# Kernel optimization log

Measured on AMD Instinct MI355X. Metric: run time of the kernel, lower is better.

Reference implementation:

```python
import jax, jax.numpy as jnp
import numpy as np

B, N, C, H = 8, 2048, 512, 8
D = C // H                      # head dim = 64
Q_LENGTHS = [1024 + 128 * i for i in range(B)]  # ragged: 1024..1920, sum below
TQ = sum(Q_LENGTHS)             # 11776 total queries


def setup_inputs() -> dict:
    key = jax.random.key(0)
    ks = jax.random.split(key, 5)
    w = 0.02  # init scale for weights
    return {
        "x": jax.random.normal(ks[0], (B, N, C), jnp.float32),
        "q": jax.random.normal(ks[1], (TQ, C), jnp.float32),
        "Wq": jax.random.normal(ks[2], (C, C), jnp.float32) * w,
        "Wkv": jax.random.normal(ks[3], (2 * C, C), jnp.float32) * w,
        "Wproj": jax.random.normal(ks[4], (C, C), jnp.float32) * w,
        "bproj": jnp.zeros((C,), jnp.float32),
        "q_lengths": jnp.array(Q_LENGTHS, jnp.int32),
        "max_q_len": max(Q_LENGTHS),
    }


def reference(x, q, Wq, Wkv, Wproj, bproj, q_lengths, max_q_len):
    # Eval path of Attention.forward: batched_sparse_attention(q, k, v, q_lengths, scale)
    # == varlen cross-attention: queries of batch b attend over all N kv tokens of batch b.
    Tq = q.shape[0]
    scale = D ** -0.5

    qh = (q @ Wq.T).reshape(Tq, H, D)                 # [Tq, H, D]
    kv = (x @ Wkv.T).reshape(B, N, 2, H, D)
    k = kv[:, :, 0]                                   # [B, N, H, D]
    v = kv[:, :, 1]                                   # [B, N, H, D]

    # ragged -> padded per-batch layout
    csum = jnp.cumsum(q_lengths)                      # [B]
    offs = jnp.concatenate([jnp.zeros((1,), csum.dtype), csum])
    tok = jnp.arange(Tq)
    q_batch = (tok[:, None] >= csum[None, :]).sum(-1)  # [Tq] batch id per query
    q_pos = tok - offs[q_batch]                        # [Tq] position within batch

    qpad = jnp.zeros((B, max_q_len, H, D), qh.dtype).at[q_batch, q_pos].set(qh)

    scores = jnp.einsum('blhd,bnhd->bhln', qpad, k) * scale  # [B, H, L, N]
    attn = jax.nn.softmax(scores, axis=-1)                   # all N keys valid
    out = jnp.einsum('bhln,bnhd->blhd', attn, v)             # [B, L, H, D]

    out = out[q_batch, q_pos].reshape(Tq, C)           # gather ragged rows back
    return out @ Wproj.T + bproj
```

## Files before the change

kernel.cpp:

```cpp
#include <hip/hip_runtime.h>
#include <hip/hip_bf16.h>
#include <math.h>

constexpr int Cc = 512;
constexpr int Hh = 8;
constexpr int Dd = 64;
constexpr int Nn = 2048;
constexpr int Bb = 8;
constexpr int GK = 512;

typedef __attribute__((ext_vector_type(8))) short short8;
typedef __attribute__((ext_vector_type(4))) float f32x4;
typedef __attribute__((ext_vector_type(4))) unsigned int u32x4;
typedef __attribute__((ext_vector_type(2))) unsigned int u32x2;

#define C2SCALE 0.1803368801f

static __device__ __forceinline__ ushort f2bf(float v) {
  __hip_bfloat16 h = __float2bfloat16(v);
  return *reinterpret_cast<ushort*>(&h);
}
static __device__ __forceinline__ float bf2f(ushort u) {
  __hip_bfloat16 h = *reinterpret_cast<__hip_bfloat16*>(&u);
  return __bfloat162float(h);
}
static __device__ __forceinline__ unsigned int pk2(float f0, float f1) {
  return (unsigned int)f2bf(f0) | ((unsigned int)f2bf(f1) << 16);
}

template <int MODE, int TERMS, bool AF32, bool BF32>
__global__ __launch_bounds__(256) void mfma_nt2_kernel(
    const void* __restrict__ A0p, const void* __restrict__ A1p,
    const void* __restrict__ B0p, const void* __restrict__ B1p,
    const float* __restrict__ bias, float* __restrict__ Cf,
    ushort* __restrict__ Chi, int Nc)
{
  __shared__ ushort lAh[128 * 32];
  __shared__ ushort lBh[128 * 32];
  __shared__ ushort lAl[TERMS == 3 ? 128 * 32 : 1];
  __shared__ ushort lBl[TERMS == 3 ? 128 * 32 : 1];

  const int tid = threadIdx.x;
  const int w = tid >> 6, lane = tid & 63;
  const int c = lane & 15, g = lane >> 4;
  const int wr = (w >> 1) * 64, wc = (w & 1) * 64;
  const int m0 = blockIdx.y * 128, n0 = blockIdx.x * 128;
  const int sr = tid >> 2;
  const int sk = (tid & 3) * 8;

  short8 rAh[2], rAl[2], rBh[2], rBl[2];

  auto ldf32 = [&](const float* F, size_t idx, short8& h, short8& l) {
    const float4 f0 = *(const float4*)(F + idx);
    const float4 f1 = *(const float4*)(F + idx + 4);
    const float vv[8] = {f0.x, f0.y, f0.z, f0.w, f1.x, f1.y, f1.z, f1.w};
#pragma unroll
    for (int j = 0; j < 8; ++j) {
      const ushort hb = f2bf(vv[j]);
      ((ushort*)&h)[j] = hb;
      if (TERMS == 3) ((ushort*)&l)[j] = f2bf(vv[j] - bf2f(hb));
    }
  };

  auto loadA = [&](int k0) {
#pragma unroll
    for (int hf = 0; hf < 2; ++hf) {
      const size_t idx = (size_t)(m0 + sr + hf * 64) * GK + k0 + sk;
      if (AF32) {
        ldf32((const float*)A0p, idx, rAh[hf], rAl[hf]);
      } else {
        rAh[hf] = *(const short8*)((const ushort*)A0p + idx);
        if (TERMS == 3) rAl[hf] = *(const short8*)((const ushort*)A1p + idx);
      }
    }
  };
  auto loadB = [&](int k0) {
#pragma unroll
    for (int hf = 0; hf < 2; ++hf) {
      const size_t idx = (size_t)(n0 + sr + hf * 64) * GK + k0 + sk;
      if (BF32) {
        ldf32((const float*)B0p, idx, rBh[hf], rBl[hf]);
      } else {
        rBh[hf] = *(const short8*)((const ushort*)B0p + idx);
        if (TERMS == 3) rBl[hf] = *(const short8*)((const ushort*)B1p + idx);
      }
    }
  };

  f32x4 acc[4][4] = {};
  loadA(0);
  loadB(0);

  for (int k0 = 0; k0 < GK; k0 += 32) {
    __syncthreads();
    *(short8*)&lAh[sr * 32 + sk]        = rAh[0];
    *(short8*)&lAh[(sr + 64) * 32 + sk] = rAh[1];
    *(short8*)&lBh[sr * 32 + sk]        = rBh[0];
    *(short8*)&lBh[(sr + 64) * 32 + sk] = rBh[1];
    if (TERMS == 3) {
      *(short8*)&lAl[sr * 32 + sk]        = rAl[0];
      *(short8*)&lAl[(sr + 64) * 32 + sk] = rAl[1];
      *(short8*)&lBl[sr * 32 + sk]        = rBl[0];
      *(short8*)&lBl[(sr + 64) * 32 + sk] = rBl[1];
    }
    __syncthreads();
    if (k0 + 32 < GK) { loadA(k0 + 32); loadB(k0 + 32); }

    short8 ah[4], al[4], bh[4], bl[4];
#pragma unroll
    for (int i = 0; i < 4; ++i) {
      const int ar = (wr + i * 16 + c) * 32 + g * 8;
      const int br = (wc + i * 16 + c) * 32 + g * 8;
      ah[i] = *(const short8*)&lAh[ar];
      bh[i] = *(const short8*)&lBh[br];
      if (TERMS == 3) {
        al[i] = *(const short8*)&lAl[ar];
        bl[i] = *(const short8*)&lBl[br];
      }
    }
#pragma unroll
    for (int mi = 0; mi < 4; ++mi)
#pragma unroll
      for (int nj = 0; nj < 4; ++nj) {
        if (TERMS == 3) {
          acc[mi][nj] = __builtin_amdgcn_mfma_f32_16x16x32_bf16(ah[mi], bl[nj], acc[mi][nj], 0,0,0);
          acc[mi][nj] = __builtin_amdgcn_mfma_f32_16x16x32_bf16(al[mi], bh[nj], acc[mi][nj], 0,0,0);
        }
        acc[mi][nj] = __builtin_amdgcn_mfma_f32_16x16x32_bf16(ah[mi], bh[nj], acc[mi][nj], 0,0,0);
      }
  }

#pragma unroll
  for (int mi = 0; mi < 4; ++mi) {
#pragma unroll
    for (int r = 0; r < 4; ++r) {
      const size_t rb = (size_t)(m0 + wr + mi * 16 + g * 4 + r) * Nc;
#pragma unroll
      for (int nj = 0; nj < 4; ++nj) {
        const int col = n0 + wc + nj * 16 + c;
        const float v = acc[mi][nj][r];
        if (MODE == 0) {
          Cf[rb + col] = v + bias[col];
        } else if (MODE == 1) {
          Chi[rb + col] = f2bf(v);
        } else {
          Chi[rb + col] = f2bf(v * C2SCALE);
        }
      }
    }
  }
}

__global__ __launch_bounds__(256, 2) void mfma_kv_fused_kernel(
    const float* __restrict__ x, const float* __restrict__ Wkv,
    ushort* __restrict__ kbf, ushort* __restrict__ vtb, int BN)
{
  __shared__ ushort smem[128 * 136];
  ushort* lA   = smem;
  ushort* lBk  = smem + 128 * 32;
  ushort* lBv  = smem + 2 * 128 * 32;
  ushort* tbuf = smem;

  const int tid = threadIdx.x;
  const int w = tid >> 6, lane = tid & 63;
  const int c = lane & 15, g = lane >> 4;
  const int wr = (w >> 1) * 64, wc = (w & 1) * 64;
  const int n0 = blockIdx.x * 128, m0 = blockIdx.y * 128;
  const int sr = tid >> 2, sk = (tid & 3) * 8;

  auto cvt8 = [&](const float* F, size_t idx) -> short8 {
    const float4 f0 = *(const float4*)(F + idx);
    const float4 f1 = *(const float4*)(F + idx + 4);
    const float vv[8] = {f0.x, f0.y, f0.z, f0.w, f1.x, f1.y, f1.z, f1.w};
    short8 h;
#pragma unroll
    for (int j = 0; j < 8; ++j) ((ushort*)&h)[j] = f2bf(vv[j]);
    return h;
  };

  short8 rA[2], rBk[2], rBv[2];
  auto loadAll = [&](int k0) {
#pragma unroll
    for (int hf = 0; hf < 2; ++hf) {
      rA[hf]  = cvt8(x,   (size_t)(m0 + sr + hf * 64) * GK + k0 + sk);
      rBk[hf] = cvt8(Wkv, (size_t)(n0 + sr + hf * 64) * GK + k0 + sk);
      rBv[hf] = cvt8(Wkv, (size_t)(512 + n0 + sr + hf * 64) * GK + k0 + sk);
    }
  };

  f32x4 ak[4][4] = {};
  f32x4 av[4][4] = {};
  loadAll(0);

  for (int k0 = 0; k0 < GK; k0 += 32) {
    __syncthreads();
    *(short8*)&lA[sr * 32 + sk]         = rA[0];
    *(short8*)&lA[(sr + 64) * 32 + sk]  = rA[1];
    *(short8*)&lBk[sr * 32 + sk]        = rBk[0];
    *(short8*)&lBk[(sr + 64) * 32 + sk] = rBk[1];
    *(short8*)&lBv[sr * 32 + sk]        = rBv[0];
    *(short8*)&lBv[(sr + 64) * 32 + sk] = rBv[1];
    __syncthreads();
    if (k0 + 32 < GK) loadAll(k0 + 32);

    short8 a[4], bk[4], bv[4];
#pragma unroll
    for (int i = 0; i < 4; ++i) {
      const int ar = (wr + i * 16 + c) * 32 + g * 8;
      const int br = (wc + i * 16 + c) * 32 + g * 8;
      a[i]  = *(const short8*)&lA[ar];
      bk[i] = *(const short8*)&lBk[br];
      bv[i] = *(const short8*)&lBv[br];
    }
#pragma unroll
    for (int mi = 0; mi < 4; ++mi)
#pragma unroll
      for (int nj = 0; nj < 4; ++nj) {
        ak[mi][nj] = __builtin_amdgcn_mfma_f32_16x16x32_bf16(a[mi], bk[nj], ak[mi][nj], 0,0,0);
        av[mi][nj] = __builtin_amdgcn_mfma_f32_16x16x32_bf16(a[mi], bv[nj], av[mi][nj], 0,0,0);
      }
  }

#pragma unroll
  for (int mi = 0; mi < 4; ++mi)
#pragma unroll
    for (int r = 0; r < 4; ++r) {
      const size_t rb = (size_t)(m0 + wr + mi * 16 + g * 4 + r) * Cc;
#pragma unroll
      for (int nj = 0; nj < 4; ++nj)
        kbf[rb + n0 + wc + nj * 16 + c] = f2bf(ak[mi][nj][r]);
    }

  __syncthreads();
#pragma unroll
  for (int mi = 0; mi < 4; ++mi)
#pragma unroll
    for (int r = 0; r < 4; ++r) {
      const int tl = wr + mi * 16 + g * 4 + r;
#pragma unroll
      for (int nj = 0; nj < 4; ++nj) {
        const int dl = wc + nj * 16 + c;
        tbuf[dl * 136 + tl] = f2bf(av[mi][nj][r]);
      }
    }
  __syncthreads();
#pragma unroll
  for (int it = 0; it < 8; ++it) {
    const int idx = tid + it * 256;
    const int row = idx >> 4;
    const int c8 = (idx & 15) * 8;
    *(short8*)&vtb[(size_t)(n0 + row) * BN + m0 + c8] =
        *(const short8*)&tbuf[row * 136 + c8];
  }
}

__global__ __launch_bounds__(256, 4) void attn_mfma12_kernel(
    const ushort* __restrict__ qhi,
    const ushort* __restrict__ kbf,
    const ushort* __restrict__ vtb,
    ushort* __restrict__ ohi,
    ushort* __restrict__ olo)
{
  constexpr int QOFF[8] = {0, 1024, 2176, 3456, 4864, 6400, 8064, 9856};

  const int lin = blockIdx.x;
  const int b  = lin & 7;
  const int h  = (lin >> 3) & 7;
  const int qt = lin >> 6;

  const int Lb  = 1024 + 128 * b;
  const int off = QOFF[b];
  if (qt * 128 >= Lb) return;

  constexpr int KP = 72;
  constexpr int VP = 136;
  constexpr int NC = Nn / 128;
  __shared__ ushort Ks[128 * KP];
  __shared__ ushort Vs[64 * VP];

  const int tid = threadIdx.x;
  const int lane = tid & 63;
  const int w = tid >> 6;
  const int c = lane & 15;
  const int g = (lane >> 4) & 3;

  short8 qf[2][2];
  int qrow[2];
#pragma unroll
  for (int t = 0; t < 2; ++t) {
    qrow[t] = off + qt * 128 + w * 32 + t * 16 + c;
    const size_t base = (size_t)qrow[t] * Cc + h * Dd + g * 8;
    qf[t][0] = *(const short8*)(qhi + base);
    qf[t][1] = *(const short8*)(qhi + base + 32);
  }

  float l_part[2] = {0.f, 0.f};
  f32x4 accO4[2][4] = {};

  const size_t kbase = (size_t)b * Nn * Cc + h * Dd;
  const size_t vbase = (size_t)h * Dd * (Bb * Nn) + (size_t)b * Nn;

  for (int ch = 0; ch < NC; ++ch) {
    __syncthreads();
#pragma unroll
    for (int it = 0; it < 4; ++it) {
      const int i = tid + it * 256;
      const int row = i >> 3, c8 = (i & 7) * 8;
      *(short8*)&Ks[row * KP + c8] =
          *(const short8*)&kbf[kbase + (size_t)(ch * 128 + row) * Cc + c8];
    }
#pragma unroll
    for (int it = 0; it < 4; ++it) {
      const int i = tid + it * 256;
      const int row = i >> 4, c8 = (i & 15) * 8;
      const int kb1 = (c8 & ~31) | (((c8 >> 3) & 3) << 2);
      const size_t gb = vbase + (size_t)row * (Bb * Nn) + ch * 128;
      const u32x2 vlo = *(const u32x2*)&vtb[gb + kb1];
      const u32x2 vhi = *(const u32x2*)&vtb[gb + kb1 + 16];
      u32x4 vv;
      vv[0] = vlo[0]; vv[1] = vlo[1];
      vv[2] = vhi[0]; vv[3] = vhi[1];
      *(short8*)&Vs[row * VP + c8] = __builtin_bit_cast(short8, vv);
    }
    __syncthreads();

#pragma unroll
    for (int st = 0; st < 2; ++st) {
      f32x4 accT4[2][4] = {};
      __builtin_amdgcn_s_setprio(1);
#pragma unroll
      for (int ks2 = 0; ks2 < 2; ++ks2) {
#pragma unroll
        for (int kb = 0; kb < 4; ++kb) {
          const short8 kf = *(const short8*)
              &Ks[(st * 64 + kb * 16 + c) * KP + ks2 * 32 + g * 8];
          accT4[0][kb] = __builtin_amdgcn_mfma_f32_16x16x32_bf16(kf, qf[0][ks2], accT4[0][kb], 0,0,0);
          accT4[1][kb] = __builtin_amdgcn_mfma_f32_16x16x32_bf16(kf, qf[1][ks2], accT4[1][kb], 0,0,0);
        }
      }
      __builtin_amdgcn_s_setprio(0);

      unsigned int up[2][4][2];
#pragma unroll
      for (int t = 0; t < 2; ++t)
#pragma unroll
        for (int kb = 0; kb < 4; ++kb) {
          const float p0 = __builtin_amdgcn_exp2f(accT4[t][kb][0]);
          const float p1 = __builtin_amdgcn_exp2f(accT4[t][kb][1]);
          const float p2 = __builtin_amdgcn_exp2f(accT4[t][kb][2]);
          const float p3 = __builtin_amdgcn_exp2f(accT4[t][kb][3]);
          l_part[t] += (p0 + p1) + (p2 + p3);
          up[t][kb][0] = pk2(p0, p1);
          up[t][kb][1] = pk2(p2, p3);
        }

#pragma unroll
      for (int ks2 = 0; ks2 < 2; ++ks2) {
        short8 pa[2];
#pragma unroll
        for (int t = 0; t < 2; ++t) {
          u32x4 wv;
          wv.x = up[t][2 * ks2][0];
          wv.y = up[t][2 * ks2][1];
          wv.z = up[t][2 * ks2 + 1][0];
          wv.w = up[t][2 * ks2 + 1][1];
          pa[t] = __builtin_bit_cast(short8, wv);
        }
        __builtin_amdgcn_s_setprio(1);
#pragma unroll
        for (int db = 0; db < 4; ++db) {
          const short8 vf = *(const short8*)
              &Vs[(db * 16 + c) * VP + st * 64 + ks2 * 32 + g * 8];
          accO4[0][db] = __builtin_amdgcn_mfma_f32_16x16x32_bf16(vf, pa[0], accO4[0][db], 0,0,0);
          accO4[1][db] = __builtin_amdgcn_mfma_f32_16x16x32_bf16(vf, pa[1], accO4[1][db], 0,0,0);
        }
        __builtin_amdgcn_s_setprio(0);
      }
    }
  }

#pragma unroll
  for (int t = 0; t < 2; ++t) {
    float l = l_part[t];
    l += __shfl_xor(l, 16);
    l += __shfl_xor(l, 32);
    const float inv = 1.f / l;
    const size_t rb = (size_t)qrow[t] * Cc + h * Dd;
#pragma unroll
    for (int db = 0; db < 4; ++db) {
      const int d0 = db * 16 + g * 4;
      ushort4 uh, ul;
#pragma unroll
      for (int e = 0; e < 4; ++e) {
        const float o = accO4[t][db][e] * inv;
        const ushort hb = f2bf(o);
        ((ushort*)&uh)[e] = hb;
        ((ushort*)&ul)[e] = f2bf(o - bf2f(hb));
      }
      *(ushort4*)&ohi[rb + d0] = uh;
      *(ushort4*)&olo[rb + d0] = ul;
    }
  }
}

extern "C" void kernel_launch(void* const* d_in, const int* in_sizes, int n_in,
                              void* d_out, int out_size, void* d_ws, size_t ws_size,
                              hipStream_t stream)
{
  const float* x     = (const float*)d_in[0];
  const float* q     = (const float*)d_in[1];
  const float* Wq    = (const float*)d_in[2];
  const float* Wkv   = (const float*)d_in[3];
  const float* Wproj = (const float*)d_in[4];
  const float* bproj = (const float*)d_in[5];

  const int TQ = in_sizes[1] / Cc;
  const int BN = in_sizes[0] / Cc;

  const size_t szQ = (size_t)TQ * Cc * 2;
  const size_t szX = (size_t)BN * Cc * 2;

  char* p = (char*)d_ws;
  ushort* q_hi  = (ushort*)p;  p += szQ;
  ushort* k_bf  = (ushort*)p;  p += szX;
  ushort* v_t   = (ushort*)p;  p += szX;
  ushort* at_hi = (ushort*)p;  p += szQ;
  ushort* at_lo = (ushort*)p;

  mfma_nt2_kernel<2, 1, true, true><<<dim3(Cc/128, TQ/128), 256, 0, stream>>>(
      q, nullptr, Wq, nullptr, nullptr, nullptr, q_hi, Cc);
  mfma_kv_fused_kernel<<<dim3(Cc/128, BN/128), 256, 0, stream>>>(
      x, Wkv, k_bf, v_t, BN);
  attn_mfma12_kernel<<<dim3(64 * 15), 256, 0, stream>>>(
      q_hi, k_bf, v_t, at_hi, at_lo);
  mfma_nt2_kernel<0, 3, false, true><<<dim3(Cc/128, TQ/128), 256, 0, stream>>>(
      at_hi, at_lo, Wproj, nullptr, bproj, (float*)d_out, nullptr, Cc);
}
```

Baseline: 174.2 us.

## Merge Q and KV projections into one launch; shrink attention KV chunk to 64

The separate Q-projection and KV-projection GEMM launches become a single kernel whose blocks pick their role from the block index. This removes one launch and lets the two independent GEMMs fill the GPU together. The attention kernel now stages K/V in 64-key chunks instead of 128, which cuts LDS per block and may allow more resident blocks, at the cost of twice as many barriers and chunk iterations. The projection GEMM template is specialized into a dedicated 3-term kernel.

```diff
diff --git a/kernel.cpp b/kernel.cpp
--- a/kernel.cpp
+++ b/kernel.cpp
@@ -28,17 +28,15 @@
   return (unsigned int)f2bf(f0) | ((unsigned int)f2bf(f1) << 16);
 }
 
-template <int MODE, int TERMS, bool AF32, bool BF32>
-__global__ __launch_bounds__(256) void mfma_nt2_kernel(
-    const void* __restrict__ A0p, const void* __restrict__ A1p,
-    const void* __restrict__ B0p, const void* __restrict__ B1p,
-    const float* __restrict__ bias, float* __restrict__ Cf,
-    ushort* __restrict__ Chi, int Nc)
+__global__ __launch_bounds__(256) void mfma_proj_kernel(
+    const ushort* __restrict__ Ah, const ushort* __restrict__ Al,
+    const float* __restrict__ Bf, const float* __restrict__ bias,
+    float* __restrict__ Cf, int Nc)
 {
   __shared__ ushort lAh[128 * 32];
   __shared__ ushort lBh[128 * 32];
-  __shared__ ushort lAl[TERMS == 3 ? 128 * 32 : 1];
-  __shared__ ushort lBl[TERMS == 3 ? 128 * 32 : 1];
+  __shared__ ushort lAl[128 * 32];
+  __shared__ ushort lBl[128 * 32];
 
   const int tid = threadIdx.x;
   const int w = tid >> 6, lane = tid & 63;
@@ -58,38 +56,23 @@
     for (int j = 0; j < 8; ++j) {
       const ushort hb = f2bf(vv[j]);
       ((ushort*)&h)[j] = hb;
-      if (TERMS == 3) ((ushort*)&l)[j] = f2bf(vv[j] - bf2f(hb));
+      ((ushort*)&l)[j] = f2bf(vv[j] - bf2f(hb));
     }
   };
 
-  auto loadA = [&](int k0) {
+  auto loadAB = [&](int k0) {
 #pragma unroll
     for (int hf = 0; hf < 2; ++hf) {
-      const size_t idx = (size_t)(m0 + sr + hf * 64) * GK + k0 + sk;
-      if (AF32) {
-        ldf32((const float*)A0p, idx, rAh[hf], rAl[hf]);
-      } else {
-        rAh[hf] = *(const short8*)((const ushort*)A0p + idx);
-        if (TERMS == 3) rAl[hf] = *(const short8*)((const ushort*)A1p + idx);
-      }
+      const size_t ia = (size_t)(m0 + sr + hf * 64) * GK + k0 + sk;
+      const size_t ib = (size_t)(n0 + sr + hf * 64) * GK + k0 + sk;
+      rAh[hf] = *(const short8*)(Ah + ia);
+      rAl[hf] = *(const short8*)(Al + ia);
+      ldf32(Bf, ib, rBh[hf], rBl[hf]);
     }
   };
-  auto loadB = [&](int k0) {
-#pragma unroll
-    for (int hf = 0; hf < 2; ++hf) {
-      const size_t idx = (size_t)(n0 + sr + hf * 64) * GK + k0 + sk;
-      if (BF32) {
-        ldf32((const float*)B0p, idx, rBh[hf], rBl[hf]);
-      } else {
-        rBh[hf] = *(const short8*)((const ushort*)B0p + idx);
-        if (TERMS == 3) rBl[hf] = *(const short8*)((const ushort*)B1p + idx);
-      }
-    }
-  };
 
   f32x4 acc[4][4] = {};
-  loadA(0);
-  loadB(0);
+  loadAB(0);
 
   for (int k0 = 0; k0 < GK; k0 += 32) {
     __syncthreads();
@@ -97,14 +80,12 @@
     *(short8*)&lAh[(sr + 64) * 32 + sk] = rAh[1];
     *(short8*)&lBh[sr * 32 + sk]        = rBh[0];
     *(short8*)&lBh[(sr + 64) * 32 + sk] = rBh[1];
-    if (TERMS == 3) {
-      *(short8*)&lAl[sr * 32 + sk]        = rAl[0];
-      *(short8*)&lAl[(sr + 64) * 32 + sk] = rAl[1];
-      *(short8*)&lBl[sr * 32 + sk]        = rBl[0];
-      *(short8*)&lBl[(sr + 64) * 32 + sk] = rBl[1];
-    }
-    __syncthreads();
-    if (k0 + 32 < GK) { loadA(k0 + 32); loadB(k0 + 32); }
+    *(short8*)&lAl[sr * 32 + sk]        = rAl[0];
+    *(short8*)&lAl[(sr + 64) * 32 + sk] = rAl[1];
+    *(short8*)&lBl[sr * 32 + sk]        = rBl[0];
+    *(short8*)&lBl[(sr + 64) * 32 + sk] = rBl[1];
+    __syncthreads();
+    if (k0 + 32 < GK) loadAB(k0 + 32);
 
     short8 ah[4], al[4], bh[4], bl[4];
 #pragma unroll
@@ -113,60 +94,47 @@
       const int br = (wc + i * 16 + c) * 32 + g * 8;
       ah[i] = *(const short8*)&lAh[ar];
       bh[i] = *(const short8*)&lBh[br];
-      if (TERMS == 3) {
-        al[i] = *(const short8*)&lAl[ar];
-        bl[i] = *(const short8*)&lBl[br];
-      }
+      al[i] = *(const short8*)&lAl[ar];
+      bl[i] = *(const short8*)&lBl[br];
     }
 #pragma unroll
     for (int mi = 0; mi < 4; ++mi)
 #pragma unroll
       for (int nj = 0; nj < 4; ++nj) {
-        if (TERMS == 3) {
-          acc[mi][nj] = __builtin_amdgcn_mfma_f32_16x16x32_bf16(ah[mi], bl[nj], acc[mi][nj], 0,0,0);
-          acc[mi][nj] = __builtin_amdgcn_mfma_f32_16x16x32_bf16(al[mi], bh[nj], acc[mi][nj], 0,0,0);
-        }
+        acc[mi][nj] = __builtin_amdgcn_mfma_f32_16x16x32_bf16(ah[mi], bl[nj], acc[mi][nj], 0,0,0);
+        acc[mi][nj] = __builtin_amdgcn_mfma_f32_16x16x32_bf16(al[mi], bh[nj], acc[mi][nj], 0,0,0);
         acc[mi][nj] = __builtin_amdgcn_mfma_f32_16x16x32_bf16(ah[mi], bh[nj], acc[mi][nj], 0,0,0);
       }
   }
 
 #pragma unroll
-  for (int mi = 0; mi < 4; ++mi) {
+  for (int mi = 0; mi < 4; ++mi)
 #pragma unroll
     for (int r = 0; r < 4; ++r) {
       const size_t rb = (size_t)(m0 + wr + mi * 16 + g * 4 + r) * Nc;
 #pragma unroll
       for (int nj = 0; nj < 4; ++nj) {
         const int col = n0 + wc + nj * 16 + c;
-        const float v = acc[mi][nj][r];
-        if (MODE == 0) {
-          Cf[rb + col] = v + bias[col];
-        } else if (MODE == 1) {
-          Chi[rb + col] = f2bf(v);
-        } else {
-          Chi[rb + col] = f2bf(v * C2SCALE);
-        }
-      }
-    }
-  }
-}
-
-__global__ __launch_bounds__(256, 2) void mfma_kv_fused_kernel(
+        Cf[rb + col] = acc[mi][nj][r] + bias[col];
+      }
+    }
+}
+
+__global__ __launch_bounds__(256, 2) void proj_qkv_kernel(
+    const float* __restrict__ qin, const float* __restrict__ Wq,
     const float* __restrict__ x, const float* __restrict__ Wkv,
-    ushort* __restrict__ kbf, ushort* __restrict__ vtb, int BN)
+    ushort* __restrict__ qhi, ushort* __restrict__ kbf,
+    ushort* __restrict__ vtb, int TQ, int BN)
 {
   __shared__ ushort smem[128 * 136];
-  ushort* lA   = smem;
-  ushort* lBk  = smem + 128 * 32;
-  ushort* lBv  = smem + 2 * 128 * 32;
-  ushort* tbuf = smem;
 
   const int tid = threadIdx.x;
   const int w = tid >> 6, lane = tid & 63;
   const int c = lane & 15, g = lane >> 4;
   const int wr = (w >> 1) * 64, wc = (w & 1) * 64;
-  const int n0 = blockIdx.x * 128, m0 = blockIdx.y * 128;
   const int sr = tid >> 2, sk = (tid & 3) * 8;
+  const int NQB = (TQ / 128) * (Cc / 128);
+  const int bid = blockIdx.x;
 
   auto cvt8 = [&](const float* F, size_t idx) -> short8 {
     const float4 f0 = *(const float4*)(F + idx);
@@ -178,83 +146,138 @@
     return h;
   };
 
-  short8 rA[2], rBk[2], rBv[2];
-  auto loadAll = [&](int k0) {
-#pragma unroll
-    for (int hf = 0; hf < 2; ++hf) {
-      rA[hf]  = cvt8(x,   (size_t)(m0 + sr + hf * 64) * GK + k0 + sk);
-      rBk[hf] = cvt8(Wkv, (size_t)(n0 + sr + hf * 64) * GK + k0 + sk);
-      rBv[hf] = cvt8(Wkv, (size_t)(512 + n0 + sr + hf * 64) * GK + k0 + sk);
-    }
-  };
-
-  f32x4 ak[4][4] = {};
-  f32x4 av[4][4] = {};
-  loadAll(0);
-
-  for (int k0 = 0; k0 < GK; k0 += 32) {
-    __syncthreads();
-    *(short8*)&lA[sr * 32 + sk]         = rA[0];
-    *(short8*)&lA[(sr + 64) * 32 + sk]  = rA[1];
-    *(short8*)&lBk[sr * 32 + sk]        = rBk[0];
-    *(short8*)&lBk[(sr + 64) * 32 + sk] = rBk[1];
-    *(short8*)&lBv[sr * 32 + sk]        = rBv[0];
-    *(short8*)&lBv[(sr + 64) * 32 + sk] = rBv[1];
-    __syncthreads();
-    if (k0 + 32 < GK) loadAll(k0 + 32);
-
-    short8 a[4], bk[4], bv[4];
-#pragma unroll
-    for (int i = 0; i < 4; ++i) {
-      const int ar = (wr + i * 16 + c) * 32 + g * 8;
-      const int br = (wc + i * 16 + c) * 32 + g * 8;
-      a[i]  = *(const short8*)&lA[ar];
-      bk[i] = *(const short8*)&lBk[br];
-      bv[i] = *(const short8*)&lBv[br];
+  if (bid < NQB) {
+    const int m0 = (bid >> 2) * 128;
+    const int n0 = (bid & 3) * 128;
+    ushort* lA = smem;
+    ushort* lB = smem + 128 * 32;
+
+    short8 rA[2], rB[2];
+    auto loadQ = [&](int k0) {
+#pragma unroll
+      for (int hf = 0; hf < 2; ++hf) {
+        rA[hf] = cvt8(qin, (size_t)(m0 + sr + hf * 64) * GK + k0 + sk);
+        rB[hf] = cvt8(Wq,  (size_t)(n0 + sr + hf * 64) * GK + k0 + sk);
+      }
+    };
+
+    f32x4 acc[4][4] = {};
+    loadQ(0);
+    for (int k0 = 0; k0 < GK; k0 += 32) {
+      __syncthreads();
+      *(short8*)&lA[sr * 32 + sk]        = rA[0];
+      *(short8*)&lA[(sr + 64) * 32 + sk] = rA[1];
+      *(short8*)&lB[sr * 32 + sk]        = rB[0];
+      *(short8*)&lB[(sr + 64) * 32 + sk] = rB[1];
+      __syncthreads();
+      if (k0 + 32 < GK) loadQ(k0 + 32);
+
+      short8 a[4], bb[4];
+#pragma unroll
+      for (int i = 0; i < 4; ++i) {
+        a[i]  = *(const short8*)&lA[(wr + i * 16 + c) * 32 + g * 8];
+        bb[i] = *(const short8*)&lB[(wc + i * 16 + c) * 32 + g * 8];
+      }
+#pragma unroll
+      for (int mi = 0; mi < 4; ++mi)
+#pragma unroll
+        for (int nj = 0; nj < 4; ++nj)
+          acc[mi][nj] = __builtin_amdgcn_mfma_f32_16x16x32_bf16(a[mi], bb[nj], acc[mi][nj], 0,0,0);
     }
 #pragma unroll
     for (int mi = 0; mi < 4; ++mi)
 #pragma unroll
-      for (int nj = 0; nj < 4; ++nj) {
-        ak[mi][nj] = __builtin_amdgcn_mfma_f32_16x16x32_bf16(a[mi], bk[nj], ak[mi][nj], 0,0,0);
-        av[mi][nj] = __builtin_amdgcn_mfma_f32_16x16x32_bf16(a[mi], bv[nj], av[mi][nj], 0,0,0);
-      }
+      for (int r = 0; r < 4; ++r) {
+        const size_t rb = (size_t)(m0 + wr + mi * 16 + g * 4 + r) * Cc;
+#pragma unroll
+        for (int nj = 0; nj < 4; ++nj)
+          qhi[rb + n0 + wc + nj * 16 + c] = f2bf(acc[mi][nj][r] * C2SCALE);
+      }
+  } else {
+    const int b2 = bid - NQB;
+    const int n0 = (b2 & 3) * 128;
+    const int m0 = (b2 >> 2) * 128;
+    ushort* lA   = smem;
+    ushort* lBk  = smem + 128 * 32;
+    ushort* lBv  = smem + 2 * 128 * 32;
+    ushort* tbuf = smem;
+
+    short8 rA[2], rBk[2], rBv[2];
+    auto loadAll = [&](int k0) {
+#pragma unroll
+      for (int hf = 0; hf < 2; ++hf) {
+        rA[hf]  = cvt8(x,   (size_t)(m0 + sr + hf * 64) * GK + k0 + sk);
+        rBk[hf] = cvt8(Wkv, (size_t)(n0 + sr + hf * 64) * GK + k0 + sk);
+        rBv[hf] = cvt8(Wkv, (size_t)(512 + n0 + sr + hf * 64) * GK + k0 + sk);
+      }
+    };
+
+    f32x4 ak[4][4] = {};
+    f32x4 av[4][4] = {};
+    loadAll(0);
+
+    for (int k0 = 0; k0 < GK; k0 += 32) {
+      __syncthreads();
+      *(short8*)&lA[sr * 32 + sk]         = rA[0];
+      *(short8*)&lA[(sr + 64) * 32 + sk]  = rA[1];
+      *(short8*)&lBk[sr * 32 + sk]        = rBk[0];
+      *(short8*)&lBk[(sr + 64) * 32 + sk] = rBk[1];
+      *(short8*)&lBv[sr * 32 + sk]        = rBv[0];
+      *(short8*)&lBv[(sr + 64) * 32 + sk] = rBv[1];
+      __syncthreads();
+      if (k0 + 32 < GK) loadAll(k0 + 32);
+
+      short8 a[4], bk[4], bv[4];
+#pragma unroll
+      for (int i = 0; i < 4; ++i) {
+        const int ar = (wr + i * 16 + c) * 32 + g * 8;
+        const int br = (wc + i * 16 + c) * 32 + g * 8;
+        a[i]  = *(const short8*)&lA[ar];
+        bk[i] = *(const short8*)&lBk[br];
+        bv[i] = *(const short8*)&lBv[br];
+      }
+#pragma unroll
+      for (int mi = 0; mi < 4; ++mi)
+#pragma unroll
+        for (int nj = 0; nj < 4; ++nj) {
+          ak[mi][nj] = __builtin_amdgcn_mfma_f32_16x16x32_bf16(a[mi], bk[nj], ak[mi][nj], 0,0,0);
+          av[mi][nj] = __builtin_amdgcn_mfma_f32_16x16x32_bf16(a[mi], bv[nj], av[mi][nj], 0,0,0);
+        }
+    }
+
+#pragma unroll
+    for (int mi = 0; mi < 4; ++mi)
+#pragma unroll
+      for (int r = 0; r < 4; ++r) {
+        const size_t rb = (size_t)(m0 + wr + mi * 16 + g * 4 + r) * Cc;
+#pragma unroll
+        for (int nj = 0; nj < 4; ++nj)
+          kbf[rb + n0 + wc + nj * 16 + c] = f2bf(ak[mi][nj][r]);
+      }
+
+    __syncthreads();
+#pragma unroll
+    for (int mi = 0; mi < 4; ++mi)
+#pragma unroll
+      for (int r = 0; r < 4; ++r) {
+        const int tl = wr + mi * 16 + g * 4 + r;
+#pragma unroll
+        for (int nj = 0; nj < 4; ++nj)
+          tbuf[(wc + nj * 16 + c) * 136 + tl] = f2bf(av[mi][nj][r]);
+      }
+    __syncthreads();
+#pragma unroll
+    for (int it = 0; it < 8; ++it) {
+      const int idx = tid + it * 256;
+      const int row = idx >> 4;
+      const int c8 = (idx & 15) * 8;
+      *(short8*)&vtb[(size_t)(n0 + row) * BN + m0 + c8] =
+          *(const short8*)&tbuf[row * 136 + c8];
+    }
   }
-
-#pragma unroll
-  for (int mi = 0; mi < 4; ++mi)
-#pragma unroll
-    for (int r = 0; r < 4; ++r) {
-      const size_t rb = (size_t)(m0 + wr + mi * 16 + g * 4 + r) * Cc;
-#pragma unroll
-      for (int nj = 0; nj < 4; ++nj)
-        kbf[rb + n0 + wc + nj * 16 + c] = f2bf(ak[mi][nj][r]);
-    }
-
-  __syncthreads();
-#pragma unroll
-  for (int mi = 0; mi < 4; ++mi)
-#pragma unroll
-    for (int r = 0; r < 4; ++r) {
-      const int tl = wr + mi * 16 + g * 4 + r;
-#pragma unroll
-      for (int nj = 0; nj < 4; ++nj) {
-        const int dl = wc + nj * 16 + c;
-        tbuf[dl * 136 + tl] = f2bf(av[mi][nj][r]);
-      }
-    }
-  __syncthreads();
-#pragma unroll
-  for (int it = 0; it < 8; ++it) {
-    const int idx = tid + it * 256;
-    const int row = idx >> 4;
-    const int c8 = (idx & 15) * 8;
-    *(short8*)&vtb[(size_t)(n0 + row) * BN + m0 + c8] =
-        *(const short8*)&tbuf[row * 136 + c8];
-  }
-}
-
-__global__ __launch_bounds__(256, 4) void attn_mfma12_kernel(
+}
+
+__global__ __launch_bounds__(256, 4) void attn_mfma14_kernel(
     const ushort* __restrict__ qhi,
     const ushort* __restrict__ kbf,
     const ushort* __restrict__ vtb,
@@ -273,10 +296,9 @@
   if (qt * 128 >= Lb) return;
 
   constexpr int KP = 72;
-  constexpr int VP = 136;
-  constexpr int NC = Nn / 128;
-  __shared__ ushort Ks[128 * KP];
-  __shared__ ushort Vs[64 * VP];
+  constexpr int NC = Nn / 64;
+  __shared__ ushort Ks[64 * KP];
+  __shared__ ushort Vs[64 * KP];
 
   const int tid = threadIdx.x;
   const int lane = tid & 63;
@@ -303,79 +325,76 @@
   for (int ch = 0; ch < NC; ++ch) {
     __syncthreads();
 #pragma unroll
-    for (int it = 0; it < 4; ++it) {
+    for (int it = 0; it < 2; ++it) {
       const int i = tid + it * 256;
       const int row = i >> 3, c8 = (i & 7) * 8;
       *(short8*)&Ks[row * KP + c8] =
-          *(const short8*)&kbf[kbase + (size_t)(ch * 128 + row) * Cc + c8];
-    }
-#pragma unroll
-    for (int it = 0; it < 4; ++it) {
+          *(const short8*)&kbf[kbase + (size_t)(ch * 64 + row) * Cc + c8];
+    }
+#pragma unroll
+    for (int it = 0; it < 2; ++it) {
       const int i = tid + it * 256;
-      const int row = i >> 4, c8 = (i & 15) * 8;
+      const int row = i >> 3, c8 = (i & 7) * 8;
       const int kb1 = (c8 & ~31) | (((c8 >> 3) & 3) << 2);
-      const size_t gb = vbase + (size_t)row * (Bb * Nn) + ch * 128;
+      const size_t gb = vbase + (size_t)row * (Bb * Nn) + ch * 64;
       const u32x2 vlo = *(const u32x2*)&vtb[gb + kb1];
       const u32x2 vhi = *(const u32x2*)&vtb[gb + kb1 + 16];
       u32x4 vv;
       vv[0] = vlo[0]; vv[1] = vlo[1];
       vv[2] = vhi[0]; vv[3] = vhi[1];
-      *(short8*)&Vs[row * VP + c8] = __builtin_bit_cast(short8, vv);
-    }
-    __syncthreads();
-
-#pragma unroll
-    for (int st = 0; st < 2; ++st) {
-      f32x4 accT4[2][4] = {};
+      *(short8*)&Vs[row * KP + c8] = __builtin_bit_cast(short8, vv);
+    }
+    __syncthreads();
+
+    f32x4 accT4[2][4] = {};
+    __builtin_amdgcn_s_setprio(1);
+#pragma unroll
+    for (int ks2 = 0; ks2 < 2; ++ks2) {
+#pragma unroll
+      for (int kb = 0; kb < 4; ++kb) {
+        const short8 kf = *(const short8*)
+            &Ks[(kb * 16 + c) * KP + ks2 * 32 + g * 8];
+        accT4[0][kb] = __builtin_amdgcn_mfma_f32_16x16x32_bf16(kf, qf[0][ks2], accT4[0][kb], 0,0,0);
+        accT4[1][kb] = __builtin_amdgcn_mfma_f32_16x16x32_bf16(kf, qf[1][ks2], accT4[1][kb], 0,0,0);
+      }
+    }
+    __builtin_amdgcn_s_setprio(0);
+
+    unsigned int up[2][4][2];
+#pragma unroll
+    for (int t = 0; t < 2; ++t)
+#pragma unroll
+      for (int kb = 0; kb < 4; ++kb) {
+        const float p0 = __builtin_amdgcn_exp2f(accT4[t][kb][0]);
+        const float p1 = __builtin_amdgcn_exp2f(accT4[t][kb][1]);
+        const float p2 = __builtin_amdgcn_exp2f(accT4[t][kb][2]);
+        const float p3 = __builtin_amdgcn_exp2f(accT4[t][kb][3]);
+        l_part[t] += (p0 + p1) + (p2 + p3);
+        up[t][kb][0] = pk2(p0, p1);
+        up[t][kb][1] = pk2(p2, p3);
+      }
+
+#pragma unroll
+    for (int ks2 = 0; ks2 < 2; ++ks2) {
+      short8 pa[2];
+#pragma unroll
+      for (int t = 0; t < 2; ++t) {
+        u32x4 wv;
+        wv.x = up[t][2 * ks2][0];
+        wv.y = up[t][2 * ks2][1];
+        wv.z = up[t][2 * ks2 + 1][0];
+        wv.w = up[t][2 * ks2 + 1][1];
+        pa[t] = __builtin_bit_cast(short8, wv);
+      }
       __builtin_amdgcn_s_setprio(1);
 #pragma unroll
-      for (int ks2 = 0; ks2 < 2; ++ks2) {
-#pragma unroll
-        for (int kb = 0; kb < 4; ++kb) {
-          const short8 kf = *(const short8*)
-              &Ks[(st * 64 + kb * 16 + c) * KP + ks2 * 32 + g * 8];
-          accT4[0][kb] = __builtin_amdgcn_mfma_f32_16x16x32_bf16(kf, qf[0][ks2], accT4[0][kb], 0,0,0);
-          accT4[1][kb] = __builtin_amdgcn_mfma_f32_16x16x32_bf16(kf, qf[1][ks2], accT4[1][kb], 0,0,0);
-        }
+      for (int db = 0; db < 4; ++db) {
+        const short8 vf = *(const short8*)
+            &Vs[(db * 16 + c) * KP + ks2 * 32 + g * 8];
+        accO4[0][db] = __builtin_amdgcn_mfma_f32_16x16x32_bf16(vf, pa[0], accO4[0][db], 0,0,0);
+        accO4[1][db] = __builtin_amdgcn_mfma_f32_16x16x32_bf16(vf, pa[1], accO4[1][db], 0,0,0);
       }
       __builtin_amdgcn_s_setprio(0);
-
-      unsigned int up[2][4][2];
-#pragma unroll
-      for (int t = 0; t < 2; ++t)
-#pragma unroll
-        for (int kb = 0; kb < 4; ++kb) {
-          const float p0 = __builtin_amdgcn_exp2f(accT4[t][kb][0]);
-          const float p1 = __builtin_amdgcn_exp2f(accT4[t][kb][1]);
-          const float p2 = __builtin_amdgcn_exp2f(accT4[t][kb][2]);
-          const float p3 = __builtin_amdgcn_exp2f(accT4[t][kb][3]);
-          l_part[t] += (p0 + p1) + (p2 + p3);
-          up[t][kb][0] = pk2(p0, p1);
-          up[t][kb][1] = pk2(p2, p3);
-        }
-
-#pragma unroll
-      for (int ks2 = 0; ks2 < 2; ++ks2) {
-        short8 pa[2];
-#pragma unroll
-        for (int t = 0; t < 2; ++t) {
-          u32x4 wv;
-          wv.x = up[t][2 * ks2][0];
-          wv.y = up[t][2 * ks2][1];
-          wv.z = up[t][2 * ks2 + 1][0];
-          wv.w = up[t][2 * ks2 + 1][1];
-          pa[t] = __builtin_bit_cast(short8, wv);
-        }
-        __builtin_amdgcn_s_setprio(1);
-#pragma unroll
-        for (int db = 0; db < 4; ++db) {
-          const short8 vf = *(const short8*)
-              &Vs[(db * 16 + c) * VP + st * 64 + ks2 * 32 + g * 8];
-          accO4[0][db] = __builtin_amdgcn_mfma_f32_16x16x32_bf16(vf, pa[0], accO4[0][db], 0,0,0);
-          accO4[1][db] = __builtin_amdgcn_mfma_f32_16x16x32_bf16(vf, pa[1], accO4[1][db], 0,0,0);
-        }
-        __builtin_amdgcn_s_setprio(0);
-      }
     }
   }
 
@@ -427,12 +446,12 @@
   ushort* at_hi = (ushort*)p;  p += szQ;
   ushort* at_lo = (ushort*)p;
 
-  mfma_nt2_kernel<2, 1, true, true><<<dim3(Cc/128, TQ/128), 256, 0, stream>>>(
-      q, nullptr, Wq, nullptr, nullptr, nullptr, q_hi, Cc);
-  mfma_kv_fused_kernel<<<dim3(Cc/128, BN/128), 256, 0, stream>>>(
-      x, Wkv, k_bf, v_t, BN);
-  attn_mfma12_kernel<<<dim3(64 * 15), 256, 0, stream>>>(
+  const int nqb = (TQ / 128) * (Cc / 128);
+  const int nkvb = (BN / 128) * (Cc / 128);
+  proj_qkv_kernel<<<dim3(nqb + nkvb), 256, 0, stream>>>(
+      q, Wq, x, Wkv, q_hi, k_bf, v_t, TQ, BN);
+  attn_mfma14_kernel<<<dim3(64 * 15), 256, 0, stream>>>(
       q_hi, k_bf, v_t, at_hi, at_lo);
-  mfma_nt2_kernel<0, 3, false, true><<<dim3(Cc/128, TQ/128), 256, 0, stream>>>(
-      at_hi, at_lo, Wproj, nullptr, bproj, (float*)d_out, nullptr, Cc);
-}
+  mfma_proj_kernel<<<dim3(Cc/128, TQ/128), 256, 0, stream>>>(
+      at_hi, at_lo, Wproj, bproj, (float*)d_out, Cc);
+}
```

Result: faster. 160.3 us, median of 3 (-8.0%).
